# Kernel optimization log

Measured on AMD Instinct MI355X. Metric: run time of the kernel, lower is better.

The kernel has to match this reference:

```python
import jax, jax.numpy as jnp
import numpy as np

N, E, F, H, A, C, NC, L, AH = 50000, 800000, 768, 256, 128, 128, 7, 2, 4

def _ln(x, g, b):
    m = jnp.mean(x, axis=-1, keepdims=True)
    v = jnp.var(x, axis=-1, keepdims=True)
    return (x - m) / jnp.sqrt(v + 1e-5) * g + b

def setup_inputs() -> dict:
    key = jax.random.key(0)
    ks = jax.random.split(key, 32)
    s = 0.02
    d = {}
    d['x'] = jax.random.normal(ks[0], (N, F), jnp.float32)
    d['edge_index'] = jax.random.randint(ks[1], (2, E), 0, N, jnp.int32)
    d['W_in'] = jax.random.normal(ks[2], (F, H), jnp.float32) * s
    d['b_in'] = jnp.zeros((H,), jnp.float32)
    d['gin_W1'] = jax.random.normal(ks[3], (L, H, H), jnp.float32) * s
    d['gin_b1'] = jnp.zeros((L, H), jnp.float32)
    d['gin_lng'] = jnp.ones((L, H), jnp.float32)
    d['gin_lnb'] = jnp.zeros((L, H), jnp.float32)
    d['gin_W2'] = jax.random.normal(ks[4], (L, H, H), jnp.float32) * s
    d['gin_b2'] = jnp.zeros((L, H), jnp.float32)
    d['eps'] = jnp.zeros((L,), jnp.float32)
    d['ln_g'] = jnp.ones((L, H), jnp.float32)
    d['ln_b'] = jnp.zeros((L, H), jnp.float32)
    d['att_W1'] = jax.random.normal(ks[5], (AH, H, A), jnp.float32) * s
    d['att_b1'] = jnp.zeros((AH, A), jnp.float32)
    d['att_W2'] = jax.random.normal(ks[6], (AH, A), jnp.float32) * s
    d['att_b2'] = jnp.zeros((AH,), jnp.float32)
    d['Wc1'] = jax.random.normal(ks[7], (H, C), jnp.float32) * s
    d['bc1'] = jnp.zeros((C,), jnp.float32)
    d['lnc1_g'] = jnp.ones((C,), jnp.float32)
    d['lnc1_b'] = jnp.zeros((C,), jnp.float32)
    d['Wc2'] = jax.random.normal(ks[8], (C, C // 2), jnp.float32) * s
    d['bc2'] = jnp.zeros((C // 2,), jnp.float32)
    d['lnc2_g'] = jnp.ones((C // 2,), jnp.float32)
    d['lnc2_b'] = jnp.zeros((C // 2,), jnp.float32)
    d['Wc3'] = jax.random.normal(ks[9], (C // 2, NC), jnp.float32) * s
    d['bc3'] = jnp.zeros((NC,), jnp.float32)
    return d

def reference(x, edge_index, W_in, b_in, gin_W1, gin_b1, gin_lng, gin_lnb, gin_W2, gin_b2, eps, ln_g, ln_b, att_W1, att_b1, att_W2, att_b2, Wc1, bc1, lnc1_g, lnc1_b, Wc2, bc2, lnc2_g, lnc2_b, Wc3, bc3):
    src, dst = edge_index[0], edge_index[1]
    # input projection (use_residual and input_dim != gnn_hidden)
    h = x @ W_in + b_in  # [N,H]
    for i in range(L):
        agg = jax.ops.segment_sum(h[src], dst, num_segments=N)  # GIN sum aggregation
        m = (1.0 + eps[i]) * h + agg
        m = _ln(m @ gin_W1[i] + gin_b1[i], gin_lng[i], gin_lnb[i])
        m = jax.nn.relu(m) @ gin_W2[i] + gin_b2[i]
        hn = jax.nn.relu(_ln(m, ln_g[i], ln_b[i]))
        h = hn + h  # residual (shapes match)
    # multi-head attention pooling, softmax over node dim
    s = jnp.tanh(jnp.einsum('nd,kda->kna', h, att_W1) + att_b1[:, None, :])  # [AH,N,A]
    logits = jnp.einsum('kna,ka->kn', s, att_W2) + att_b2[:, None]  # [AH,N]
    a = jax.nn.softmax(logits, axis=1)  # [AH,N]
    z = jnp.einsum('kn,nd->kd', a, h)  # [AH,H]
    z_agg = jnp.mean(z, axis=0)  # [H]
    attn = a.T  # [N,AH]
    # classifier (full variant)
    c = jax.nn.relu(_ln(z_agg @ Wc1 + bc1, lnc1_g, lnc1_b))
    c = jax.nn.relu(_ln(c @ Wc2 + bc2, lnc2_g, lnc2_b))
    probs = jax.nn.softmax(c @ Wc3 + bc3, axis=0)
    return probs, attn
```

## Files before the change

### kernel.cpp

```cpp
#include <hip/hip_runtime.h>
#include <math.h>

#define NN 50000
#define NE 800000
#define FF 768
#define HH 256

typedef __attribute__((ext_vector_type(8))) short short8;
typedef __attribute__((ext_vector_type(4))) float f32x4;

__device__ inline unsigned short f2bf(float f) {
  unsigned u = __float_as_uint(f);
  u = u + 0x7fffu + ((u >> 16) & 1u);
  return (unsigned short)(u >> 16);
}
__device__ inline float bf2f(unsigned short b) {
  return __uint_as_float(((unsigned)b) << 16);
}

__global__ void k_count(const int* __restrict__ dstv, int* __restrict__ deg) {
  int e = blockIdx.x * 256 + threadIdx.x;
  if (e < NE) atomicAdd(&deg[dstv[e]], 1);
}

__global__ void k_scan(const int* __restrict__ deg, int* __restrict__ rowptr) {
  const int CH = 49;
  int tid = threadIdx.x;
  int lane = tid & 63, w = tid >> 6;
  int base = tid * CH;
  int sum = 0;
  for (int i = 0; i < CH; i++) {
    int idx = base + i;
    if (idx < NN) sum += deg[idx];
  }
  int incl = sum;
  for (int off = 1; off < 64; off <<= 1) {
    int tv = __shfl_up(incl, off, 64);
    if (lane >= off) incl += tv;
  }
  __shared__ int ws[16];
  if (lane == 63) ws[w] = incl;
  __syncthreads();
  if (tid == 0) {
    int c = 0;
    for (int i = 0; i < 16; i++) { int tv = ws[i]; ws[i] = c; c += tv; }
  }
  __syncthreads();
  int run = ws[w] + (incl - sum);
  if (tid == 0) rowptr[0] = 0;
  for (int i = 0; i < CH; i++) {
    int idx = base + i;
    if (idx < NN) { run += deg[idx]; rowptr[idx + 1] = run; }
  }
}

__global__ void k_scatter(const int* __restrict__ srcv, const int* __restrict__ dstv,
                          int* __restrict__ cursor, int* __restrict__ csr_src) {
  int e = blockIdx.x * 256 + threadIdx.x;
  if (e < NE) {
    int d = dstv[e];
    int pos = atomicAdd(&cursor[d], 1);
    csr_src[pos] = srcv[e];
  }
}

__global__ void k_agg(const unsigned short* __restrict__ hb, const int* __restrict__ rowptr,
                      const int* __restrict__ csr_src, const float* __restrict__ eps,
                      int layer, unsigned short* __restrict__ mb) {
  int node = (blockIdx.x * blockDim.x + threadIdx.x) >> 6;
  int lane = threadIdx.x & 63;
  if (node >= NN) return;
  int beg = rowptr[node], end = rowptr[node + 1];
  const ushort4* hv = (const ushort4*)hb;
  float ax = 0.f, ay = 0.f, az = 0.f, aw = 0.f;
  for (int e = beg; e < end; ++e) {
    int s = csr_src[e];
    ushort4 v = hv[(size_t)s * 64 + lane];
    ax += bf2f(v.x); ay += bf2f(v.y); az += bf2f(v.z); aw += bf2f(v.w);
  }
  float ep = 1.0f + eps[layer];
  ushort4 h0 = hv[(size_t)node * 64 + lane];
  ax += ep * bf2f(h0.x); ay += ep * bf2f(h0.y);
  az += ep * bf2f(h0.z); aw += ep * bf2f(h0.w);
  ushort4 o;
  o.x = f2bf(ax); o.y = f2bf(ay); o.z = f2bf(az); o.w = f2bf(aw);
  *(ushort4*)&mb[(size_t)node * 256 + lane * 4] = o;
}

__global__ void k_tcast(const float* __restrict__ src, unsigned short* __restrict__ dst,
                        int R, int C) {
  __shared__ float tile[32][33];
  int bx = blockIdx.x * 32, by = blockIdx.y * 32;
  int tx = threadIdx.x & 31, ty = threadIdx.x >> 5;
  for (int i = 0; i < 32; i += 8) {
    int r = by + ty + i, c = bx + tx;
    tile[ty + i][tx] = (r < R && c < C) ? src[(size_t)r * C + c] : 0.f;
  }
  __syncthreads();
  for (int i = 0; i < 32; i += 8) {
    int c = bx + ty + i, r = by + tx;
    if (c < C && r < R) dst[(size_t)c * R + r] = f2bf(tile[tx][ty + i]);
  }
}

template <int KTOT, int EPI, bool AF32, bool WF>
__global__ __launch_bounds__(256) void k_mm(
    const void* __restrict__ Ap, const unsigned short* __restrict__ Bt,
    const float* __restrict__ bias, const float* __restrict__ g,
    const float* __restrict__ be, const float* __restrict__ resid,
    float* __restrict__ outf, unsigned short* __restrict__ outb) {
  __shared__ unsigned short As[64 * 40];
  __shared__ unsigned short Bs[256 * 40];
  __shared__ float redS[4][64];
  __shared__ float redQ[4][64];
  __shared__ float mvM[64], mvI[64];
  int t = threadIdx.x, lane = t & 63, wave = t >> 6;
  int row0 = blockIdx.x * 64;
  f32x4 acc[4][4];
#pragma unroll
  for (int i = 0; i < 4; i++)
#pragma unroll
    for (int j = 0; j < 4; j++) acc[i][j] = (f32x4)(0.f);
  int arow = t >> 2, ac = t & 3;
  int agr = row0 + arow; if (agr >= NN) agr = NN - 1;
  int m16 = lane & 15, kq = lane >> 4;

  for (int k0 = 0; k0 < KTOT; k0 += 32) {
    if (AF32) {
      const float* Af = (const float*)Ap + (size_t)agr * KTOT + k0 + ac * 8;
      float4 f0 = *(const float4*)Af;
      float4 f1 = *(const float4*)(Af + 4);
      short8 v;
      v[0] = (short)f2bf(f0.x); v[1] = (short)f2bf(f0.y);
      v[2] = (short)f2bf(f0.z); v[3] = (short)f2bf(f0.w);
      v[4] = (short)f2bf(f1.x); v[5] = (short)f2bf(f1.y);
      v[6] = (short)f2bf(f1.z); v[7] = (short)f2bf(f1.w);
      *(short8*)&As[arow * 40 + ac * 8] = v;
    } else {
      const unsigned short* Ab = (const unsigned short*)Ap + (size_t)agr * KTOT + k0 + ac * 8;
      *(float4*)&As[arow * 40 + ac * 8] = *(const float4*)Ab;
    }
#pragma unroll
    for (int it = 0; it < 4; it++) {
      int idx = t + it * 256;
      int br = idx >> 2, bc = idx & 3;
      *(float4*)&Bs[br * 40 + bc * 8] = *(const float4*)&Bt[(size_t)br * KTOT + k0 + bc * 8];
    }
    __syncthreads();
    short8 a[4], b[4];
#pragma unroll
    for (int rt = 0; rt < 4; rt++) a[rt] = *(const short8*)&As[(rt * 16 + m16) * 40 + kq * 8];
#pragma unroll
    for (int ct = 0; ct < 4; ct++)
      b[ct] = *(const short8*)&Bs[(wave * 64 + ct * 16 + m16) * 40 + kq * 8];
#pragma unroll
    for (int rt = 0; rt < 4; rt++)
#pragma unroll
      for (int ct = 0; ct < 4; ct++)
        acc[rt][ct] = __builtin_amdgcn_mfma_f32_16x16x32_bf16(a[rt], b[ct], acc[rt][ct], 0, 0, 0);
    __syncthreads();
  }

  int colbase = wave * 64 + m16;
  float bv[4];
#pragma unroll
  for (int ct = 0; ct < 4; ct++) bv[ct] = bias[colbase + ct * 16];

  if (EPI == 0) {
#pragma unroll
    for (int rt = 0; rt < 4; rt++)
#pragma unroll
      for (int reg = 0; reg < 4; reg++) {
        int r = row0 + rt * 16 + kq * 4 + reg;
        if (r < NN) {
#pragma unroll
          for (int ct = 0; ct < 4; ct++) {
            float v = acc[rt][ct][reg] + bv[ct];
            outf[(size_t)r * 256 + colbase + ct * 16] = v;
            outb[(size_t)r * 256 + colbase + ct * 16] = f2bf(v);
          }
        }
      }
    return;
  }

  float s[4][4], q[4][4];
#pragma unroll
  for (int rt = 0; rt < 4; rt++)
#pragma unroll
    for (int reg = 0; reg < 4; reg++) { s[rt][reg] = 0.f; q[rt][reg] = 0.f; }
#pragma unroll
  for (int rt = 0; rt < 4; rt++)
#pragma unroll
    for (int ct = 0; ct < 4; ct++)
#pragma unroll
      for (int reg = 0; reg < 4; reg++) {
        float v = acc[rt][ct][reg] + bv[ct];
        acc[rt][ct][reg] = v;
        s[rt][reg] += v;
        q[rt][reg] += v * v;
      }
#pragma unroll
  for (int off = 1; off < 16; off <<= 1) {
#pragma unroll
    for (int rt = 0; rt < 4; rt++)
#pragma unroll
      for (int reg = 0; reg < 4; reg++) {
        s[rt][reg] += __shfl_xor(s[rt][reg], off, 64);
        q[rt][reg] += __shfl_xor(q[rt][reg], off, 64);
      }
  }
  if (m16 == 0) {
#pragma unroll
    for (int rt = 0; rt < 4; rt++)
#pragma unroll
      for (int reg = 0; reg < 4; reg++) {
        redS[wave][rt * 16 + kq * 4 + reg] = s[rt][reg];
        redQ[wave][rt * 16 + kq * 4 + reg] = q[rt][reg];
      }
  }
  __syncthreads();
  if (t < 64) {
    float ss = redS[0][t] + redS[1][t] + redS[2][t] + redS[3][t];
    float qq = redQ[0][t] + redQ[1][t] + redQ[2][t] + redQ[3][t];
    float mean = ss * (1.f / 256.f);
    float var = qq * (1.f / 256.f) - mean * mean;
    mvM[t] = mean;
    mvI[t] = rsqrtf(var + 1e-5f);
  }
  __syncthreads();
  float gv[4], bev[4];
#pragma unroll
  for (int ct = 0; ct < 4; ct++) { gv[ct] = g[colbase + ct * 16]; bev[ct] = be[colbase + ct * 16]; }
#pragma unroll
  for (int rt = 0; rt < 4; rt++)
#pragma unroll
    for (int reg = 0; reg < 4; reg++) {
      int rr = rt * 16 + kq * 4 + reg;
      int r = row0 + rr;
      if (r >= NN) continue;
      float mean = mvM[rr], inv = mvI[rr];
#pragma unroll
      for (int ct = 0; ct < 4; ct++) {
        int col = colbase + ct * 16;
        float val = fmaxf((acc[rt][ct][reg] - mean) * inv * gv[ct] + bev[ct], 0.f);
        if (EPI == 2) {
          val += resid[(size_t)r * 256 + col];
          if (WF) outf[(size_t)r * 256 + col] = val;
        }
        outb[(size_t)r * 256 + col] = f2bf(val);
      }
    }
}

__global__ __launch_bounds__(256) void k_att(const unsigned short* __restrict__ hb,
    const unsigned short* __restrict__ W1T, const float* __restrict__ b1,
    const float* __restrict__ W2, const float* __restrict__ b2,
    float* __restrict__ logitsT) {
  __shared__ unsigned short As[64 * 40];
  __shared__ unsigned short Bs[512 * 40];
  int t = threadIdx.x, lane = t & 63, wave = t >> 6;
  int row0 = blockIdx.x * 64;
  f32x4 acc[4][8];
#pragma unroll
  for (int i = 0; i < 4; i++)
#pragma unroll
    for (int j = 0; j < 8; j++) acc[i][j] = (f32x4)(0.f);
  int arow = t >> 2, ac = t & 3;
  int agr = row0 + arow; if (agr >= NN) agr = NN - 1;
  int m16 = lane & 15, kq = lane >> 4;
  for (int k0 = 0; k0 < 256; k0 += 32) {
    *(float4*)&As[arow * 40 + ac * 8] = *(const float4*)&hb[(size_t)agr * 256 + k0 + ac * 8];
#pragma unroll
    for (int it = 0; it < 8; it++) {
      int idx = t + it * 256;
      int br = idx >> 2, bc = idx & 3;
      *(float4*)&Bs[br * 40 + bc * 8] = *(const float4*)&W1T[(size_t)br * 256 + k0 + bc * 8];
    }
    __syncthreads();
    short8 a[4];
#pragma unroll
    for (int rt = 0; rt < 4; rt++) a[rt] = *(const short8*)&As[(rt * 16 + m16) * 40 + kq * 8];
#pragma unroll
    for (int ct = 0; ct < 8; ct++) {
      short8 b = *(const short8*)&Bs[(wave * 128 + ct * 16 + m16) * 40 + kq * 8];
#pragma unroll
      for (int rt = 0; rt < 4; rt++)
        acc[rt][ct] = __builtin_amdgcn_mfma_f32_16x16x32_bf16(a[rt], b, acc[rt][ct], 0, 0, 0);
    }
    __syncthreads();
  }
  const float* b1k = b1 + wave * 128;
  const float* w2k = W2 + wave * 128;
  float p[4][4];
#pragma unroll
  for (int rt = 0; rt < 4; rt++)
#pragma unroll
    for (int reg = 0; reg < 4; reg++) p[rt][reg] = 0.f;
#pragma unroll
  for (int ct = 0; ct < 8; ct++) {
    int col = ct * 16 + m16;
    float b1v = b1k[col], w2v = w2k[col];
#pragma unroll
    for (int rt = 0; rt < 4; rt++)
#pragma unroll
      for (int reg = 0; reg < 4; reg++) {
        float xv = acc[rt][ct][reg] + b1v;
        xv = fminf(fmaxf(xv, -10.f), 10.f);
        float ex = __expf(2.f * xv);
        p[rt][reg] += (ex - 1.f) / (ex + 1.f) * w2v;
      }
  }
#pragma unroll
  for (int off = 1; off < 16; off <<= 1)
#pragma unroll
    for (int rt = 0; rt < 4; rt++)
#pragma unroll
      for (int reg = 0; reg < 4; reg++) p[rt][reg] += __shfl_xor(p[rt][reg], off, 64);
  if (m16 == 0) {
    float b2v = b2[wave];
#pragma unroll
    for (int rt = 0; rt < 4; rt++)
#pragma unroll
      for (int reg = 0; reg < 4; reg++) {
        int r = row0 + rt * 16 + kq * 4 + reg;
        if (r < NN) logitsT[(size_t)wave * NN + r] = p[rt][reg] + b2v;
      }
  }
}

__global__ void k_smax1(const float* __restrict__ logitsT, float* __restrict__ pmax,
                        float* __restrict__ psum) {
  int k = blockIdx.y;
  int tid = threadIdx.x;
  const float* L = logitsT + (size_t)k * NN;
  __shared__ float sm[256];
  float mx = -1e30f;
  for (int i = blockIdx.x * 256 + tid; i < NN; i += 128 * 256) mx = fmaxf(mx, L[i]);
  sm[tid] = mx; __syncthreads();
  for (int o = 128; o >= 1; o >>= 1) { if (tid < o) sm[tid] = fmaxf(sm[tid], sm[tid + o]); __syncthreads(); }
  float bmax = sm[0];
  __syncthreads();
  float s = 0.f;
  for (int i = blockIdx.x * 256 + tid; i < NN; i += 128 * 256) s += __expf(L[i] - bmax);
  sm[tid] = s; __syncthreads();
  for (int o = 128; o >= 1; o >>= 1) { if (tid < o) sm[tid] += sm[tid + o]; __syncthreads(); }
  if (tid == 0) { pmax[k * 128 + blockIdx.x] = bmax; psum[k * 128 + blockIdx.x] = sm[0]; }
}

__global__ void k_smax2(const float* __restrict__ pmax, const float* __restrict__ psum,
                        float* __restrict__ gs) {
  int k = blockIdx.x;
  int tid = threadIdx.x;
  __shared__ float sm[128], sv[128];
  float m = pmax[k * 128 + tid];
  sm[tid] = m; __syncthreads();
  for (int o = 64; o >= 1; o >>= 1) { if (tid < o) sm[tid] = fmaxf(sm[tid], sm[tid + o]); __syncthreads(); }
  float gm = sm[0];
  __syncthreads();
  sv[tid] = psum[k * 128 + tid] * __expf(m - gm);
  __syncthreads();
  for (int o = 64; o >= 1; o >>= 1) { if (tid < o) sv[tid] += sv[tid + o]; __syncthreads(); }
  if (tid == 0) { gs[k * 2] = gm; gs[k * 2 + 1] = sv[0]; }
}

__global__ void k_attnz(const float* __restrict__ logitsT, const float* __restrict__ gs,
                        const unsigned short* __restrict__ hb, float* __restrict__ out_attn,
                        float* __restrict__ z) {
  int n0 = blockIdx.x * 128;
  int tid = threadIdx.x;
  __shared__ float a[4][128];
  for (int i = tid; i < 512; i += 256) {
    int k = i >> 7, n = i & 127;
    float v = 0.f;
    if (n0 + n < NN) v = __expf(logitsT[(size_t)k * NN + n0 + n] - gs[k * 2]) / gs[k * 2 + 1];
    a[k][n] = v;
  }
  __syncthreads();
  for (int i = tid; i < 512; i += 256) {
    int n = i >> 2, k = i & 3;
    if (n0 + n < NN) out_attn[(size_t)(n0 + n) * 4 + k] = a[k][n];
  }
  float z0 = 0.f, z1 = 0.f, z2 = 0.f, z3 = 0.f;
  int d = tid;
  int nmax = NN - n0; if (nmax > 128) nmax = 128;
  for (int n = 0; n < nmax; n++) {
    float hv = bf2f(hb[(size_t)(n0 + n) * 256 + d]);
    z0 += a[0][n] * hv; z1 += a[1][n] * hv; z2 += a[2][n] * hv; z3 += a[3][n] * hv;
  }
  atomicAdd(&z[0 * 256 + d], z0);
  atomicAdd(&z[1 * 256 + d], z1);
  atomicAdd(&z[2 * 256 + d], z2);
  atomicAdd(&z[3 * 256 + d], z3);
}

__global__ void k_cls(const float* __restrict__ z, const float* __restrict__ Wc1,
                      const float* __restrict__ bc1, const float* __restrict__ g1,
                      const float* __restrict__ b1, const float* __restrict__ Wc2,
                      const float* __restrict__ bc2, const float* __restrict__ g2,
                      const float* __restrict__ b2, const float* __restrict__ Wc3,
                      const float* __restrict__ bc3, float* __restrict__ out) {
  int tid = threadIdx.x;
  __shared__ float za[256];
  __shared__ float buf[256];
  __shared__ float c1s[128];
  __shared__ float c2s[64];
  za[tid] = 0.25f * (z[tid] + z[256 + tid] + z[512 + tid] + z[768 + tid]);
  __syncthreads();
  float v1 = 0.f;
  if (tid < 128) {
    for (int d = 0; d < 256; d++) v1 += za[d] * Wc1[d * 128 + tid];
    v1 += bc1[tid];
  }
  buf[tid] = (tid < 128) ? v1 : 0.f; __syncthreads();
  for (int o = 128; o >= 1; o >>= 1) { if (tid < o) buf[tid] += buf[tid + o]; __syncthreads(); }
  float mean1 = buf[0] * (1.f / 128.f);
  __syncthreads();
  buf[tid] = (tid < 128) ? (v1 - mean1) * (v1 - mean1) : 0.f; __syncthreads();
  for (int o = 128; o >= 1; o >>= 1) { if (tid < o) buf[tid] += buf[tid + o]; __syncthreads(); }
  float inv1 = rsqrtf(buf[0] * (1.f / 128.f) + 1e-5f);
  __syncthreads();
  if (tid < 128) c1s[tid] = fmaxf((v1 - mean1) * inv1 * g1[tid] + b1[tid], 0.f);
  __syncthreads();
  float v2 = 0.f;
  if (tid < 64) {
    for (int d = 0; d < 128; d++) v2 += c1s[d] * Wc2[d * 64 + tid];
    v2 += bc2[tid];
  }
  buf[tid] = (tid < 64) ? v2 : 0.f; __syncthreads();
  for (int o = 128; o >= 1; o >>= 1) { if (tid < o) buf[tid] += buf[tid + o]; __syncthreads(); }
  float mean2 = buf[0] * (1.f / 64.f);
  __syncthreads();
  buf[tid] = (tid < 64) ? (v2 - mean2) * (v2 - mean2) : 0.f; __syncthreads();
  for (int o = 128; o >= 1; o >>= 1) { if (tid < o) buf[tid] += buf[tid + o]; __syncthreads(); }
  float inv2 = rsqrtf(buf[0] * (1.f / 64.f) + 1e-5f);
  __syncthreads();
  if (tid < 64) c2s[tid] = fmaxf((v2 - mean2) * inv2 * g2[tid] + b2[tid], 0.f);
  __syncthreads();
  if (tid < 7) {
    float l = 0.f;
    for (int d = 0; d < 64; d++) l += c2s[d] * Wc3[d * 7 + tid];
    buf[tid] = l + bc3[tid];
  }
  __syncthreads();
  if (tid == 0) {
    float mx = -1e30f;
    for (int i = 0; i < 7; i++) mx = fmaxf(mx, buf[i]);
    float s = 0.f;
    for (int i = 0; i < 7; i++) s += __expf(buf[i] - mx);
    for (int i = 0; i < 7; i++) out[i] = __expf(buf[i] - mx) / s;
  }
}

extern "C" void kernel_launch(void* const* d_in, const int* in_sizes, int n_in,
                              void* d_out, int out_size, void* d_ws, size_t ws_size,
                              hipStream_t stream) {
  const float* x       = (const float*)d_in[0];
  const int*   ei      = (const int*)d_in[1];
  const float* W_in    = (const float*)d_in[2];
  const float* b_in    = (const float*)d_in[3];
  const float* gin_W1  = (const float*)d_in[4];
  const float* gin_b1  = (const float*)d_in[5];
  const float* gin_lng = (const float*)d_in[6];
  const float* gin_lnb = (const float*)d_in[7];
  const float* gin_W2  = (const float*)d_in[8];
  const float* gin_b2  = (const float*)d_in[9];
  const float* eps     = (const float*)d_in[10];
  const float* ln_g    = (const float*)d_in[11];
  const float* ln_b    = (const float*)d_in[12];
  const float* att_W1  = (const float*)d_in[13];
  const float* att_b1  = (const float*)d_in[14];
  const float* att_W2  = (const float*)d_in[15];
  const float* att_b2  = (const float*)d_in[16];
  const float* Wc1     = (const float*)d_in[17];
  const float* bc1     = (const float*)d_in[18];
  const float* lnc1_g  = (const float*)d_in[19];
  const float* lnc1_b  = (const float*)d_in[20];
  const float* Wc2     = (const float*)d_in[21];
  const float* bc2     = (const float*)d_in[22];
  const float* lnc2_g  = (const float*)d_in[23];
  const float* lnc2_b  = (const float*)d_in[24];
  const float* Wc3     = (const float*)d_in[25];
  const float* bc3     = (const float*)d_in[26];
  float* out = (float*)d_out;
  (void)in_sizes; (void)n_in; (void)out_size; (void)ws_size;

  char* wsb = (char*)d_ws;
  size_t off = 0;
  auto alloc = [&](size_t bytes) {
    char* p = wsb + off;
    off += (bytes + 255) & ~(size_t)255;
    return p;
  };
  float*          h       = (float*)alloc((size_t)NN * HH * 4);
  unsigned short* hb      = (unsigned short*)alloc((size_t)NN * HH * 2);
  unsigned short* mb1     = (unsigned short*)alloc((size_t)NN * HH * 2);
  unsigned short* mb2     = (unsigned short*)alloc((size_t)NN * HH * 2);
  unsigned short* WinT    = (unsigned short*)alloc((size_t)HH * FF * 2);
  unsigned short* g1T     = (unsigned short*)alloc((size_t)2 * HH * HH * 2);
  unsigned short* g2T     = (unsigned short*)alloc((size_t)2 * HH * HH * 2);
  unsigned short* aW1T    = (unsigned short*)alloc((size_t)4 * 128 * HH * 2);
  float*          logitsT = (float*)alloc((size_t)4 * NN * 4);
  int*            deg     = (int*)alloc((size_t)NN * 4);
  int*            rowptr  = (int*)alloc((size_t)(NN + 1) * 4);
  int*            cursor  = (int*)alloc((size_t)NN * 4);
  int*            csr_src = (int*)alloc((size_t)NE * 4);
  float*          pmax    = (float*)alloc(4 * 128 * 4);
  float*          psum    = (float*)alloc(4 * 128 * 4);
  float*          gs      = (float*)alloc(8 * 4);
  float*          z       = (float*)alloc(4 * 256 * 4);

  const int* srcv = ei;
  const int* dstv = ei + NE;

  k_tcast<<<dim3((HH + 31) / 32, (FF + 31) / 32), 256, 0, stream>>>(W_in, WinT, FF, HH);
  for (int l = 0; l < 2; l++) {
    k_tcast<<<dim3(8, 8), 256, 0, stream>>>(gin_W1 + (size_t)l * HH * HH, g1T + (size_t)l * HH * HH, HH, HH);
    k_tcast<<<dim3(8, 8), 256, 0, stream>>>(gin_W2 + (size_t)l * HH * HH, g2T + (size_t)l * HH * HH, HH, HH);
  }
  for (int kh = 0; kh < 4; kh++)
    k_tcast<<<dim3(4, 8), 256, 0, stream>>>(att_W1 + (size_t)kh * HH * 128, aW1T + (size_t)kh * 128 * HH, HH, 128);

  hipMemsetAsync(deg, 0, (size_t)NN * 4, stream);
  hipMemsetAsync(z, 0, 4 * 256 * 4, stream);
  k_count<<<(NE + 255) / 256, 256, 0, stream>>>(dstv, deg);
  k_scan<<<1, 1024, 0, stream>>>(deg, rowptr);
  hipMemcpyAsync(cursor, rowptr, (size_t)NN * 4, hipMemcpyDeviceToDevice, stream);
  k_scatter<<<(NE + 255) / 256, 256, 0, stream>>>(srcv, dstv, cursor, csr_src);

  int gblocks = (NN + 63) / 64;
  k_mm<FF, 0, true, true><<<gblocks, 256, 0, stream>>>(x, WinT, b_in, nullptr, nullptr, nullptr, h, hb);

  for (int l = 0; l < 2; l++) {
    k_agg<<<(NN + 3) / 4, 256, 0, stream>>>(hb, rowptr, csr_src, eps, l, mb1);
    k_mm<HH, 1, false, true><<<gblocks, 256, 0, stream>>>(mb1, g1T + (size_t)l * HH * HH,
        gin_b1 + l * HH, gin_lng + l * HH, gin_lnb + l * HH, nullptr, nullptr, mb2);
    if (l == 0)
      k_mm<HH, 2, false, true><<<gblocks, 256, 0, stream>>>(mb2, g2T + (size_t)l * HH * HH,
          gin_b2 + l * HH, ln_g + l * HH, ln_b + l * HH, h, h, hb);
    else
      k_mm<HH, 2, false, false><<<gblocks, 256, 0, stream>>>(mb2, g2T + (size_t)l * HH * HH,
          gin_b2 + l * HH, ln_g + l * HH, ln_b + l * HH, h, nullptr, hb);
  }

  k_att<<<gblocks, 256, 0, stream>>>(hb, aW1T, att_b1, att_W2, att_b2, logitsT);
  k_smax1<<<dim3(128, 4), 256, 0, stream>>>(logitsT, pmax, psum);
  k_smax2<<<4, 128, 0, stream>>>(pmax, psum, gs);
  k_attnz<<<(NN + 127) / 128, 256, 0, stream>>>(logitsT, gs, hb, out + 7, z);
  k_cls<<<1, 256, 0, stream>>>(z, Wc1, bc1, lnc1_g, lnc1_b, Wc2, bc2, lnc2_g, lnc2_b,
                               Wc3, bc3, out);
}
```

Baseline: 957.4 us.

## Stage full A row-tile in LDS and read weights directly from global

The GEMM kernels (input projection, GIN MLPs, attention) now load the whole 64x256 bf16 activation tile into shared memory once, with no per-k-step barriers. B-operand weight fragments are read straight from global/L2 instead of being staged through LDS. The weight transpose launches are also batched using blockIdx.z. This removes per-iteration syncs and LDS staging of weights, but relies on cache hits for the repeated weight reads and uses more LDS per block, which can lower occupancy.

After: 1.010 ms. 5.5% more time.

```diff
diff --git a/kernel.cpp b/kernel.cpp
--- a/kernel.cpp
+++ b/kernel.cpp
@@ -87,8 +87,10 @@
   *(ushort4*)&mb[(size_t)node * 256 + lane * 4] = o;
 }
 
-__global__ void k_tcast(const float* __restrict__ src, unsigned short* __restrict__ dst,
+__global__ void k_tcast(const float* __restrict__ src0, unsigned short* __restrict__ dst0,
                         int R, int C) {
+  const float* src = src0 + (size_t)blockIdx.z * R * C;
+  unsigned short* dst = dst0 + (size_t)blockIdx.z * R * C;
   __shared__ float tile[32][33];
   int bx = blockIdx.x * 32, by = blockIdx.y * 32;
   int tx = threadIdx.x & 31, ty = threadIdx.x >> 5;
@@ -103,86 +105,121 @@
   }
 }
 
-template <int KTOT, int EPI, bool AF32, bool WF>
-__global__ __launch_bounds__(256) void k_mm(
-    const void* __restrict__ Ap, const unsigned short* __restrict__ Bt,
+__global__ __launch_bounds__(256) void k_mmff(
+    const float* __restrict__ x, const unsigned short* __restrict__ Bt,
+    const float* __restrict__ bias, float* __restrict__ outf,
+    unsigned short* __restrict__ outb) {
+  __shared__ unsigned short As[64 * 264];
+  int t = threadIdx.x, lane = t & 63, wave = t >> 6;
+  int row0 = blockIdx.x * 64;
+  int m16 = lane & 15, kq = lane >> 4;
+  f32x4 acc[4][4];
+#pragma unroll
+  for (int i = 0; i < 4; i++)
+#pragma unroll
+    for (int j = 0; j < 4; j++) acc[i][j] = (f32x4)(0.f);
+  int sr = t >> 5;
+  int sc = (t & 31) * 8;
+
+  for (int kc = 0; kc < FF; kc += 256) {
+    if (kc) __syncthreads();
+#pragma unroll
+    for (int j = 0; j < 8; j++) {
+      int rr = j * 8 + sr;
+      int gr = row0 + rr; if (gr >= NN) gr = NN - 1;
+      const float* xp = x + (size_t)gr * FF + kc + sc;
+      float4 f0 = *(const float4*)xp;
+      float4 f1 = *(const float4*)(xp + 4);
+      short8 v;
+      v[0] = (short)f2bf(f0.x); v[1] = (short)f2bf(f0.y);
+      v[2] = (short)f2bf(f0.z); v[3] = (short)f2bf(f0.w);
+      v[4] = (short)f2bf(f1.x); v[5] = (short)f2bf(f1.y);
+      v[6] = (short)f2bf(f1.z); v[7] = (short)f2bf(f1.w);
+      *(short8*)&As[rr * 264 + sc] = v;
+    }
+    __syncthreads();
+#pragma unroll
+    for (int k0 = 0; k0 < 256; k0 += 32) {
+      short8 a[4], b[4];
+#pragma unroll
+      for (int rt = 0; rt < 4; rt++)
+        a[rt] = *(const short8*)&As[(rt * 16 + m16) * 264 + k0 + kq * 8];
+#pragma unroll
+      for (int ct = 0; ct < 4; ct++)
+        b[ct] = *(const short8*)&Bt[(size_t)(wave * 64 + ct * 16 + m16) * FF + kc + k0 + kq * 8];
+#pragma unroll
+      for (int rt = 0; rt < 4; rt++)
+#pragma unroll
+        for (int ct = 0; ct < 4; ct++)
+          acc[rt][ct] = __builtin_amdgcn_mfma_f32_16x16x32_bf16(a[rt], b[ct], acc[rt][ct], 0, 0, 0);
+    }
+  }
+  int colbase = wave * 64 + m16;
+  float bv[4];
+#pragma unroll
+  for (int ct = 0; ct < 4; ct++) bv[ct] = bias[colbase + ct * 16];
+#pragma unroll
+  for (int rt = 0; rt < 4; rt++)
+#pragma unroll
+    for (int reg = 0; reg < 4; reg++) {
+      int r = row0 + rt * 16 + kq * 4 + reg;
+      if (r < NN) {
+#pragma unroll
+        for (int ct = 0; ct < 4; ct++) {
+          float v = acc[rt][ct][reg] + bv[ct];
+          outf[(size_t)r * 256 + colbase + ct * 16] = v;
+          outb[(size_t)r * 256 + colbase + ct * 16] = f2bf(v);
+        }
+      }
+    }
+}
+
+template <int EPI, bool WF>
+__global__ __launch_bounds__(256) void k_mmh(
+    const unsigned short* __restrict__ Ab, const unsigned short* __restrict__ Bt,
     const float* __restrict__ bias, const float* __restrict__ g,
     const float* __restrict__ be, const float* __restrict__ resid,
     float* __restrict__ outf, unsigned short* __restrict__ outb) {
-  __shared__ unsigned short As[64 * 40];
-  __shared__ unsigned short Bs[256 * 40];
+  __shared__ unsigned short As[64 * 264];
   __shared__ float redS[4][64];
   __shared__ float redQ[4][64];
   __shared__ float mvM[64], mvI[64];
   int t = threadIdx.x, lane = t & 63, wave = t >> 6;
   int row0 = blockIdx.x * 64;
+  int sr = t >> 5, sc = (t & 31) * 8;
+#pragma unroll
+  for (int j = 0; j < 8; j++) {
+    int rr = j * 8 + sr;
+    int gr = row0 + rr; if (gr >= NN) gr = NN - 1;
+    *(float4*)&As[rr * 264 + sc] = *(const float4*)&Ab[(size_t)gr * 256 + sc];
+  }
+  __syncthreads();
+  int m16 = lane & 15, kq = lane >> 4;
   f32x4 acc[4][4];
 #pragma unroll
   for (int i = 0; i < 4; i++)
 #pragma unroll
     for (int j = 0; j < 4; j++) acc[i][j] = (f32x4)(0.f);
-  int arow = t >> 2, ac = t & 3;
-  int agr = row0 + arow; if (agr >= NN) agr = NN - 1;
-  int m16 = lane & 15, kq = lane >> 4;
-
-  for (int k0 = 0; k0 < KTOT; k0 += 32) {
-    if (AF32) {
-      const float* Af = (const float*)Ap + (size_t)agr * KTOT + k0 + ac * 8;
-      float4 f0 = *(const float4*)Af;
-      float4 f1 = *(const float4*)(Af + 4);
-      short8 v;
-      v[0] = (short)f2bf(f0.x); v[1] = (short)f2bf(f0.y);
-      v[2] = (short)f2bf(f0.z); v[3] = (short)f2bf(f0.w);
-      v[4] = (short)f2bf(f1.x); v[5] = (short)f2bf(f1.y);
-      v[6] = (short)f2bf(f1.z); v[7] = (short)f2bf(f1.w);
-      *(short8*)&As[arow * 40 + ac * 8] = v;
-    } else {
-      const unsigned short* Ab = (const unsigned short*)Ap + (size_t)agr * KTOT + k0 + ac * 8;
-      *(float4*)&As[arow * 40 + ac * 8] = *(const float4*)Ab;
-    }
-#pragma unroll
-    for (int it = 0; it < 4; it++) {
-      int idx = t + it * 256;
-      int br = idx >> 2, bc = idx & 3;
-      *(float4*)&Bs[br * 40 + bc * 8] = *(const float4*)&Bt[(size_t)br * KTOT + k0 + bc * 8];
-    }
-    __syncthreads();
+#pragma unroll
+  for (int k0 = 0; k0 < 256; k0 += 32) {
     short8 a[4], b[4];
 #pragma unroll
-    for (int rt = 0; rt < 4; rt++) a[rt] = *(const short8*)&As[(rt * 16 + m16) * 40 + kq * 8];
+    for (int rt = 0; rt < 4; rt++)
+      a[rt] = *(const short8*)&As[(rt * 16 + m16) * 264 + k0 + kq * 8];
 #pragma unroll
     for (int ct = 0; ct < 4; ct++)
-      b[ct] = *(const short8*)&Bs[(wave * 64 + ct * 16 + m16) * 40 + kq * 8];
+      b[ct] = *(const short8*)&Bt[(size_t)(wave * 64 + ct * 16 + m16) * 256 + k0 + kq * 8];
 #pragma unroll
     for (int rt = 0; rt < 4; rt++)
 #pragma unroll
       for (int ct = 0; ct < 4; ct++)
         acc[rt][ct] = __builtin_amdgcn_mfma_f32_16x16x32_bf16(a[rt], b[ct], acc[rt][ct], 0, 0, 0);
-    __syncthreads();
   }
 
   int colbase = wave * 64 + m16;
   float bv[4];
 #pragma unroll
   for (int ct = 0; ct < 4; ct++) bv[ct] = bias[colbase + ct * 16];
-
-  if (EPI == 0) {
-#pragma unroll
-    for (int rt = 0; rt < 4; rt++)
-#pragma unroll
-      for (int reg = 0; reg < 4; reg++) {
-        int r = row0 + rt * 16 + kq * 4 + reg;
-        if (r < NN) {
-#pragma unroll
-          for (int ct = 0; ct < 4; ct++) {
-            float v = acc[rt][ct][reg] + bv[ct];
-            outf[(size_t)r * 256 + colbase + ct * 16] = v;
-            outb[(size_t)r * 256 + colbase + ct * 16] = f2bf(v);
-          }
-        }
-      }
-    return;
-  }
 
   float s[4][4], q[4][4];
 #pragma unroll
@@ -257,38 +294,36 @@
     const unsigned short* __restrict__ W1T, const float* __restrict__ b1,
     const float* __restrict__ W2, const float* __restrict__ b2,
     float* __restrict__ logitsT) {
-  __shared__ unsigned short As[64 * 40];
-  __shared__ unsigned short Bs[512 * 40];
+  __shared__ unsigned short As[64 * 264];
   int t = threadIdx.x, lane = t & 63, wave = t >> 6;
   int row0 = blockIdx.x * 64;
+  int sr = t >> 5, sc = (t & 31) * 8;
+#pragma unroll
+  for (int j = 0; j < 8; j++) {
+    int rr = j * 8 + sr;
+    int gr = row0 + rr; if (gr >= NN) gr = NN - 1;
+    *(float4*)&As[rr * 264 + sc] = *(const float4*)&hb[(size_t)gr * 256 + sc];
+  }
+  __syncthreads();
+  int m16 = lane & 15, kq = lane >> 4;
   f32x4 acc[4][8];
 #pragma unroll
   for (int i = 0; i < 4; i++)
 #pragma unroll
     for (int j = 0; j < 8; j++) acc[i][j] = (f32x4)(0.f);
-  int arow = t >> 2, ac = t & 3;
-  int agr = row0 + arow; if (agr >= NN) agr = NN - 1;
-  int m16 = lane & 15, kq = lane >> 4;
+#pragma unroll
   for (int k0 = 0; k0 < 256; k0 += 32) {
-    *(float4*)&As[arow * 40 + ac * 8] = *(const float4*)&hb[(size_t)agr * 256 + k0 + ac * 8];
-#pragma unroll
-    for (int it = 0; it < 8; it++) {
-      int idx = t + it * 256;
-      int br = idx >> 2, bc = idx & 3;
-      *(float4*)&Bs[br * 40 + bc * 8] = *(const float4*)&W1T[(size_t)br * 256 + k0 + bc * 8];
-    }
-    __syncthreads();
     short8 a[4];
 #pragma unroll
-    for (int rt = 0; rt < 4; rt++) a[rt] = *(const short8*)&As[(rt * 16 + m16) * 40 + kq * 8];
+    for (int rt = 0; rt < 4; rt++)
+      a[rt] = *(const short8*)&As[(rt * 16 + m16) * 264 + k0 + kq * 8];
 #pragma unroll
     for (int ct = 0; ct < 8; ct++) {
-      short8 b = *(const short8*)&Bs[(wave * 128 + ct * 16 + m16) * 40 + kq * 8];
+      short8 b = *(const short8*)&W1T[(size_t)(wave * 128 + ct * 16 + m16) * 256 + k0 + kq * 8];
 #pragma unroll
       for (int rt = 0; rt < 4; rt++)
         acc[rt][ct] = __builtin_amdgcn_mfma_f32_16x16x32_bf16(a[rt], b, acc[rt][ct], 0, 0, 0);
     }
-    __syncthreads();
   }
   const float* b1k = b1 + wave * 128;
   const float* w2k = W2 + wave * 128;
@@ -513,13 +548,10 @@
   const int* srcv = ei;
   const int* dstv = ei + NE;
 
-  k_tcast<<<dim3((HH + 31) / 32, (FF + 31) / 32), 256, 0, stream>>>(W_in, WinT, FF, HH);
-  for (int l = 0; l < 2; l++) {
-    k_tcast<<<dim3(8, 8), 256, 0, stream>>>(gin_W1 + (size_t)l * HH * HH, g1T + (size_t)l * HH * HH, HH, HH);
-    k_tcast<<<dim3(8, 8), 256, 0, stream>>>(gin_W2 + (size_t)l * HH * HH, g2T + (size_t)l * HH * HH, HH, HH);
-  }
-  for (int kh = 0; kh < 4; kh++)
-    k_tcast<<<dim3(4, 8), 256, 0, stream>>>(att_W1 + (size_t)kh * HH * 128, aW1T + (size_t)kh * 128 * HH, HH, 128);
+  k_tcast<<<dim3((HH + 31) / 32, (FF + 31) / 32, 1), 256, 0, stream>>>(W_in, WinT, FF, HH);
+  k_tcast<<<dim3(8, 8, 2), 256, 0, stream>>>(gin_W1, g1T, HH, HH);
+  k_tcast<<<dim3(8, 8, 2), 256, 0, stream>>>(gin_W2, g2T, HH, HH);
+  k_tcast<<<dim3(4, 8, 4), 256, 0, stream>>>(att_W1, aW1T, HH, 128);
 
   hipMemsetAsync(deg, 0, (size_t)NN * 4, stream);
   hipMemsetAsync(z, 0, 4 * 256 * 4, stream);
@@ -529,17 +561,17 @@
   k_scatter<<<(NE + 255) / 256, 256, 0, stream>>>(srcv, dstv, cursor, csr_src);
 
   int gblocks = (NN + 63) / 64;
-  k_mm<FF, 0, true, true><<<gblocks, 256, 0, stream>>>(x, WinT, b_in, nullptr, nullptr, nullptr, h, hb);
+  k_mmff<<<gblocks, 256, 0, stream>>>(x, WinT, b_in, h, hb);
 
   for (int l = 0; l < 2; l++) {
     k_agg<<<(NN + 3) / 4, 256, 0, stream>>>(hb, rowptr, csr_src, eps, l, mb1);
-    k_mm<HH, 1, false, true><<<gblocks, 256, 0, stream>>>(mb1, g1T + (size_t)l * HH * HH,
+    k_mmh<1, true><<<gblocks, 256, 0, stream>>>(mb1, g1T + (size_t)l * HH * HH,
         gin_b1 + l * HH, gin_lng + l * HH, gin_lnb + l * HH, nullptr, nullptr, mb2);
     if (l == 0)
-      k_mm<HH, 2, false, true><<<gblocks, 256, 0, stream>>>(mb2, g2T + (size_t)l * HH * HH,
+      k_mmh<2, true><<<gblocks, 256, 0, stream>>>(mb2, g2T + (size_t)l * HH * HH,
           gin_b2 + l * HH, ln_g + l * HH, ln_b + l * HH, h, h, hb);
     else
-      k_mm<HH, 2, false, false><<<gblocks, 256, 0, stream>>>(mb2, g2T + (size_t)l * HH * HH,
+      k_mmh<2, false><<<gblocks, 256, 0, stream>>>(mb2, g2T + (size_t)l * HH * HH,
           gin_b2 + l * HH, ln_g + l * HH, ln_b + l * HH, h, nullptr, hb);
   }
 
```

## Use direct global-to-LDS loads with XOR swizzle and batch weight transposes

Applied to the files above, without the earlier changes.

GEMM and attention kernels now stage bf16 tiles with global_load_lds (direct global-to-LDS DMA) instead of loading through registers. The padded 40-element LDS rows become unpadded 32-element rows with an XOR swizzle to avoid bank conflicts. Weight transpose launches are merged into fewer launches using blockIdx.z. This is meant to cut VGPR pressure, instruction count and launch overhead, but the swizzle indexing and the wave-contiguous LDS destination layout have to match exactly.

After: 935.2 us. 1.02x faster.

```diff
diff --git a/kernel.cpp b/kernel.cpp
--- a/kernel.cpp
+++ b/kernel.cpp
@@ -16,6 +16,12 @@
 }
 __device__ inline float bf2f(unsigned short b) {
   return __uint_as_float(((unsigned)b) << 16);
+}
+
+__device__ __forceinline__ void ldsload16(const unsigned short* g, unsigned short* l) {
+  __builtin_amdgcn_global_load_lds(
+      (const __attribute__((address_space(1))) void*)g,
+      (__attribute__((address_space(3))) void*)l, 16, 0, 0);
 }
 
 __global__ void k_count(const int* __restrict__ dstv, int* __restrict__ deg) {
@@ -87,8 +93,10 @@
   *(ushort4*)&mb[(size_t)node * 256 + lane * 4] = o;
 }
 
-__global__ void k_tcast(const float* __restrict__ src, unsigned short* __restrict__ dst,
+__global__ void k_tcast(const float* __restrict__ src0, unsigned short* __restrict__ dst0,
                         int R, int C) {
+  const float* src = src0 + (size_t)blockIdx.z * R * C;
+  unsigned short* dst = dst0 + (size_t)blockIdx.z * R * C;
   __shared__ float tile[32][33];
   int bx = blockIdx.x * 32, by = blockIdx.y * 32;
   int tx = threadIdx.x & 31, ty = threadIdx.x >> 5;
@@ -109,8 +117,8 @@
     const float* __restrict__ bias, const float* __restrict__ g,
     const float* __restrict__ be, const float* __restrict__ resid,
     float* __restrict__ outf, unsigned short* __restrict__ outb) {
-  __shared__ unsigned short As[64 * 40];
-  __shared__ unsigned short Bs[256 * 40];
+  __shared__ unsigned short As[64 * 32];
+  __shared__ unsigned short Bs[256 * 32];
   __shared__ float redS[4][64];
   __shared__ float redQ[4][64];
   __shared__ float mvM[64], mvI[64];
@@ -121,13 +129,23 @@
   for (int i = 0; i < 4; i++)
 #pragma unroll
     for (int j = 0; j < 4; j++) acc[i][j] = (f32x4)(0.f);
-  int arow = t >> 2, ac = t & 3;
+  int m16 = lane & 15, kq = lane >> 4;
+
+  int arow = t >> 2, a2 = t & 3;
+  int asl = a2 ^ (arow & 3);
   int agr = row0 + arow; if (agr >= NN) agr = NN - 1;
-  int m16 = lane & 15, kq = lane >> 4;
+  unsigned short* AsDst = &As[wave * 512];
+  int brow_[4], bsl_[4];
+#pragma unroll
+  for (int j = 0; j < 4; j++) {
+    int s = j * 256 + t;
+    brow_[j] = s >> 2;
+    bsl_[j] = (s & 3) ^ (brow_[j] & 3);
+  }
 
   for (int k0 = 0; k0 < KTOT; k0 += 32) {
     if (AF32) {
-      const float* Af = (const float*)Ap + (size_t)agr * KTOT + k0 + ac * 8;
+      const float* Af = (const float*)Ap + (size_t)agr * KTOT + k0 + asl * 8;
       float4 f0 = *(const float4*)Af;
       float4 f1 = *(const float4*)(Af + 4);
       short8 v;
@@ -135,24 +153,26 @@
       v[2] = (short)f2bf(f0.z); v[3] = (short)f2bf(f0.w);
       v[4] = (short)f2bf(f1.x); v[5] = (short)f2bf(f1.y);
       v[6] = (short)f2bf(f1.z); v[7] = (short)f2bf(f1.w);
-      *(short8*)&As[arow * 40 + ac * 8] = v;
+      *(short8*)&As[arow * 32 + a2 * 8] = v;
     } else {
-      const unsigned short* Ab = (const unsigned short*)Ap + (size_t)agr * KTOT + k0 + ac * 8;
-      *(float4*)&As[arow * 40 + ac * 8] = *(const float4*)Ab;
+      ldsload16((const unsigned short*)Ap + (size_t)agr * KTOT + k0 + asl * 8, AsDst);
     }
 #pragma unroll
-    for (int it = 0; it < 4; it++) {
-      int idx = t + it * 256;
-      int br = idx >> 2, bc = idx & 3;
-      *(float4*)&Bs[br * 40 + bc * 8] = *(const float4*)&Bt[(size_t)br * KTOT + k0 + bc * 8];
-    }
+    for (int j = 0; j < 4; j++)
+      ldsload16(&Bt[(size_t)brow_[j] * KTOT + k0 + bsl_[j] * 8],
+                &Bs[(j * 256 + wave * 64) * 8]);
     __syncthreads();
     short8 a[4], b[4];
 #pragma unroll
-    for (int rt = 0; rt < 4; rt++) a[rt] = *(const short8*)&As[(rt * 16 + m16) * 40 + kq * 8];
-#pragma unroll
-    for (int ct = 0; ct < 4; ct++)
-      b[ct] = *(const short8*)&Bs[(wave * 64 + ct * 16 + m16) * 40 + kq * 8];
+    for (int rt = 0; rt < 4; rt++) {
+      int row = rt * 16 + m16;
+      a[rt] = *(const short8*)&As[row * 32 + ((kq ^ (row & 3)) * 8)];
+    }
+#pragma unroll
+    for (int ct = 0; ct < 4; ct++) {
+      int row = wave * 64 + ct * 16 + m16;
+      b[ct] = *(const short8*)&Bs[row * 32 + ((kq ^ (row & 3)) * 8)];
+    }
 #pragma unroll
     for (int rt = 0; rt < 4; rt++)
 #pragma unroll
@@ -257,8 +277,8 @@
     const unsigned short* __restrict__ W1T, const float* __restrict__ b1,
     const float* __restrict__ W2, const float* __restrict__ b2,
     float* __restrict__ logitsT) {
-  __shared__ unsigned short As[64 * 40];
-  __shared__ unsigned short Bs[512 * 40];
+  __shared__ unsigned short As[64 * 32];
+  __shared__ unsigned short Bs[512 * 32];
   int t = threadIdx.x, lane = t & 63, wave = t >> 6;
   int row0 = blockIdx.x * 64;
   f32x4 acc[4][8];
@@ -266,24 +286,35 @@
   for (int i = 0; i < 4; i++)
 #pragma unroll
     for (int j = 0; j < 8; j++) acc[i][j] = (f32x4)(0.f);
-  int arow = t >> 2, ac = t & 3;
+  int m16 = lane & 15, kq = lane >> 4;
+  int arow = t >> 2, a2 = t & 3;
+  int asl = a2 ^ (arow & 3);
   int agr = row0 + arow; if (agr >= NN) agr = NN - 1;
-  int m16 = lane & 15, kq = lane >> 4;
+  unsigned short* AsDst = &As[wave * 512];
+  int brow_[8], bsl_[8];
+#pragma unroll
+  for (int j = 0; j < 8; j++) {
+    int s = j * 256 + t;
+    brow_[j] = s >> 2;
+    bsl_[j] = (s & 3) ^ (brow_[j] & 3);
+  }
   for (int k0 = 0; k0 < 256; k0 += 32) {
-    *(float4*)&As[arow * 40 + ac * 8] = *(const float4*)&hb[(size_t)agr * 256 + k0 + ac * 8];
-#pragma unroll
-    for (int it = 0; it < 8; it++) {
-      int idx = t + it * 256;
-      int br = idx >> 2, bc = idx & 3;
-      *(float4*)&Bs[br * 40 + bc * 8] = *(const float4*)&W1T[(size_t)br * 256 + k0 + bc * 8];
-    }
+    ldsload16(&hb[(size_t)agr * 256 + k0 + asl * 8], AsDst);
+#pragma unroll
+    for (int j = 0; j < 8; j++)
+      ldsload16(&W1T[(size_t)brow_[j] * 256 + k0 + bsl_[j] * 8],
+                &Bs[(j * 256 + wave * 64) * 8]);
     __syncthreads();
     short8 a[4];
 #pragma unroll
-    for (int rt = 0; rt < 4; rt++) a[rt] = *(const short8*)&As[(rt * 16 + m16) * 40 + kq * 8];
+    for (int rt = 0; rt < 4; rt++) {
+      int row = rt * 16 + m16;
+      a[rt] = *(const short8*)&As[row * 32 + ((kq ^ (row & 3)) * 8)];
+    }
 #pragma unroll
     for (int ct = 0; ct < 8; ct++) {
-      short8 b = *(const short8*)&Bs[(wave * 128 + ct * 16 + m16) * 40 + kq * 8];
+      int row = wave * 128 + ct * 16 + m16;
+      short8 b = *(const short8*)&Bs[row * 32 + ((kq ^ (row & 3)) * 8)];
 #pragma unroll
       for (int rt = 0; rt < 4; rt++)
         acc[rt][ct] = __builtin_amdgcn_mfma_f32_16x16x32_bf16(a[rt], b, acc[rt][ct], 0, 0, 0);
@@ -513,13 +544,10 @@
   const int* srcv = ei;
   const int* dstv = ei + NE;
 
-  k_tcast<<<dim3((HH + 31) / 32, (FF + 31) / 32), 256, 0, stream>>>(W_in, WinT, FF, HH);
-  for (int l = 0; l < 2; l++) {
-    k_tcast<<<dim3(8, 8), 256, 0, stream>>>(gin_W1 + (size_t)l * HH * HH, g1T + (size_t)l * HH * HH, HH, HH);
-    k_tcast<<<dim3(8, 8), 256, 0, stream>>>(gin_W2 + (size_t)l * HH * HH, g2T + (size_t)l * HH * HH, HH, HH);
-  }
-  for (int kh = 0; kh < 4; kh++)
-    k_tcast<<<dim3(4, 8), 256, 0, stream>>>(att_W1 + (size_t)kh * HH * 128, aW1T + (size_t)kh * 128 * HH, HH, 128);
+  k_tcast<<<dim3((HH + 31) / 32, (FF + 31) / 32, 1), 256, 0, stream>>>(W_in, WinT, FF, HH);
+  k_tcast<<<dim3(8, 8, 2), 256, 0, stream>>>(gin_W1, g1T, HH, HH);
+  k_tcast<<<dim3(8, 8, 2), 256, 0, stream>>>(gin_W2, g2T, HH, HH);
+  k_tcast<<<dim3(4, 8, 4), 256, 0, stream>>>(att_W1, aW1T, HH, 128);
 
   hipMemsetAsync(deg, 0, (size_t)NN * 4, stream);
   hipMemsetAsync(z, 0, 4 * 256 * 4, stream);
```
